# Performance work log

Hardware: AMD Instinct MI355X
Metric: run time of the kernel (lower is better)

## Reference

```python
import jax, jax.numpy as jnp
import numpy as np

B, S, D, F, V, R = 4, 1024, 768, 3072, 2048, 8


def setup_inputs() -> dict:
    key = jax.random.key(0)
    k_x, k_r, k_w1, k_b1, k_w2, k_b2 = jax.random.split(key, 6)
    e_two = jax.random.normal(k_x, (B, S, D), dtype=jnp.float32)
    route_ids = jax.random.randint(k_r, (B, S), 0, R, dtype=jnp.int32)
    # Per-route classification head params (stacked over route axis R).
    W1 = jax.random.normal(k_w1, (R, D, F), dtype=jnp.float32) / np.sqrt(D)
    b1 = jnp.zeros((R, F), dtype=jnp.float32)
    W2 = jax.random.normal(k_w2, (R, F, V), dtype=jnp.float32) / np.sqrt(F)
    b2 = jnp.zeros((R, V), dtype=jnp.float32)
    return {"e_two": e_two, "route_ids": route_ids,
            "W1": W1, "b1": b1, "W2": W2, "b2": b2}


def reference(e_two, route_ids, W1, b1, W2, b2):
    # Each token goes through the MLP classification head selected by its
    # route_id:  softmax(relu(x @ W1[r] + b1[r]) @ W2[r] + b2[r]).
    # Dense formulation: run every route head over all tokens (R is a small
    # fixed set), then gather each token's own route output.
    h = jax.nn.relu(jnp.einsum('bsd,rdf->rbsf', e_two, W1)
                    + b1[:, None, None, :])            # [R,B,S,F]
    logits_all = jnp.einsum('rbsf,rfv->rbsv', h, W2) + b2[:, None, None, :]
    # Select per-token route: [R,B,S,V] -> [B,S,R,V] -> gather along R.
    logits_all = jnp.moveaxis(logits_all, 0, 2)        # [B,S,R,V]
    idx = route_ids[:, :, None, None].astype(jnp.int32)  # [B,S,1,1]
    logits = jnp.take_along_axis(logits_all, idx, axis=2)[:, :, 0, :]  # [B,S,V]
    return jax.nn.softmax(logits, axis=-1)
```

## Files before the change

### kernel.cpp

```cpp
#include <hip/hip_runtime.h>


typedef __attribute__((ext_vector_type(8))) short    s16x8;
typedef __attribute__((ext_vector_type(4))) float    f32x4;

#define T_TOK 4096
#define D_    768
#define F_    3072
#define V_    2048
#define R_    8
#define BM    128
#define BN    128
#define BK    64
#define MAXTILES 40
#define PADROWS  5120

#define OFF_COUNTS  ((size_t)0)
#define OFF_CURS    ((size_t)64)
#define OFF_PADOFF  ((size_t)128)
#define OFF_NT      ((size_t)192)
#define OFF_TROUTE  ((size_t)256)
#define OFF_TROW    ((size_t)1024)
#define OFF_TOK     ((size_t)4096)
#define OFF_XG      ((size_t)32768)
#define OFF_H       (OFF_XG  + (size_t)PADROWS*D_*2)
#define OFF_W1T     (OFF_H   + (size_t)PADROWS*F_*2)
#define OFF_W2T     (OFF_W1T + (size_t)R_*F_*D_*2)

static __device__ __forceinline__ unsigned short f2bf(float f) {
  union { float f; unsigned int u; } x; x.f = f;
  unsigned int r = x.u + 0x7FFFu + ((x.u >> 16) & 1u);
  return (unsigned short)(r >> 16);
}

static __device__ __forceinline__ void gload_lds16(const unsigned short* g,
                                                   unsigned short* l) {
  __builtin_amdgcn_global_load_lds(
      (const __attribute__((address_space(1))) unsigned int*)(const void*)g,
      (__attribute__((address_space(3))) unsigned int*)(void*)l, 16, 0, 0);
}

__global__ void cr_count(const int* __restrict__ route, int* __restrict__ counts) {
  int t = blockIdx.x * blockDim.x + threadIdx.x;
  if (t < T_TOK) atomicAdd(&counts[route[t]], 1);
}

__global__ void cr_plan(const int* __restrict__ counts, int* __restrict__ padOff,
                        int* __restrict__ nTiles, int* __restrict__ tRoute,
                        int* __restrict__ tRow) {
  if (threadIdx.x != 0 || blockIdx.x != 0) return;
  int off = 0, tiles = 0;
  for (int r = 0; r < R_; ++r) {
    padOff[r] = off;
    int nt = (counts[r] + BM - 1) / BM;
    for (int i = 0; i < nt; ++i) { tRoute[tiles] = r; tRow[tiles] = off + i * BM; ++tiles; }
    off += nt * BM;
  }
  padOff[R_] = off;
  *nTiles = tiles;
}

__global__ void cr_scatter(const float* __restrict__ X, const int* __restrict__ route,
                           const int* __restrict__ padOff, int* __restrict__ curs,
                           int* __restrict__ tok, unsigned short* __restrict__ Xg) {
  __shared__ int spos;
  int t = blockIdx.x;
  if (threadIdx.x == 0) {
    int r = route[t];
    int p = padOff[r] + atomicAdd(&curs[r], 1);
    tok[p] = t;
    spos = p;
  }
  __syncthreads();
  int pos = spos;
  float4 v = reinterpret_cast<const float4*>(X + (size_t)t * D_)[threadIdx.x];
  ushort4 o;
  o.x = f2bf(v.x); o.y = f2bf(v.y); o.z = f2bf(v.z); o.w = f2bf(v.w);
  *reinterpret_cast<ushort4*>(Xg + (size_t)pos * D_ + threadIdx.x * 4) = o;
}

template <int K, int N>
__global__ void cr_transpose(const float* __restrict__ W, unsigned short* __restrict__ Wt) {
  __shared__ float tile[128][65];
  int r = blockIdx.z;
  const float* Wr = W + (size_t)r * K * N;
  unsigned short* Wtr = Wt + (size_t)r * N * K;
  int k0 = blockIdx.x * 128, n0 = blockIdx.y * 64;
  int t = threadIdx.x;
  int cb = (t & 15) * 4, rb = t >> 4;
#pragma unroll
  for (int i = 0; i < 8; ++i) {
    int k = rb + i * 16;
    float4 v = *reinterpret_cast<const float4*>(Wr + (size_t)(k0 + k) * N + n0 + cb);
    tile[k][cb] = v.x; tile[k][cb + 1] = v.y; tile[k][cb + 2] = v.z; tile[k][cb + 3] = v.w;
  }
  __syncthreads();
  int nl = t >> 3, kc = (t & 7) * 16;
#pragma unroll
  for (int np = 0; np < 2; ++np) {
    int n = nl + np * 32;
    alignas(16) unsigned short o[16];
#pragma unroll
    for (int j = 0; j < 16; ++j) o[j] = f2bf(tile[kc + j][n]);
    unsigned short* dst = Wtr + (size_t)(n0 + n) * K + k0 + kc;
    *reinterpret_cast<s16x8*>(dst)     = *reinterpret_cast<const s16x8*>(&o[0]);
    *reinterpret_cast<s16x8*>(dst + 8) = *reinterpret_cast<const s16x8*>(&o[8]);
  }
}

template <int K, int N, int MODE, int KSLICES>
__global__ __launch_bounds__(256) void cr_gemm(
    const unsigned short* __restrict__ A, const unsigned short* __restrict__ Wt,
    const float* __restrict__ bias, const int* __restrict__ nTiles,
    const int* __restrict__ tRoute, const int* __restrict__ tRow,
    const int* __restrict__ tok, unsigned short* __restrict__ Hout,
    float* __restrict__ Fout) {
  constexpr int NY = N / BN;
  constexpr int KS_LEN = K / KSLICES;
  int bid = blockIdx.x;
  int ks  = bid / (MAXTILES * NY);
  int rem = bid - ks * (MAXTILES * NY);
  int y   = rem / MAXTILES;
  int mt  = rem - y * MAXTILES;
  if (mt >= *nTiles) return;
  int route = tRoute[mt], row0 = tRow[mt];
  int col0 = y * BN;
  int kbase = ks * KS_LEN;
  const unsigned short* Ag = A + (size_t)row0 * K + kbase;
  const unsigned short* Bg = Wt + ((size_t)route * N + col0) * K + kbase;

  __shared__ __align__(16) unsigned short As[BM * BK];
  __shared__ __align__(16) unsigned short Bs[BN * BK];

  int tid = threadIdx.x, lane = tid & 63, w = tid >> 6;
  int wr = w >> 1, wc = w & 1;
  int rl = lane >> 3;
  int kx = ((lane & 7) ^ rl) * 8;
  int frow = lane & 15;
  int fk   = (lane >> 4) * 8;
  int rx   = (frow & 7) << 3;

  f32x4 acc[4][4] = {};

  for (int kt = 0; kt < KS_LEN; kt += BK) {
#pragma unroll
    for (int j = 0; j < 4; ++j) {
      int c = j * 4 + w;
      gload_lds16(Ag + (size_t)(c * 8 + rl) * K + kt + kx, As + c * 512);
    }
#pragma unroll
    for (int j = 0; j < 4; ++j) {
      int c = j * 4 + w;
      gload_lds16(Bg + (size_t)(c * 8 + rl) * K + kt + kx, Bs + c * 512);
    }
    __syncthreads();
#pragma unroll
    for (int kk = 0; kk < 2; ++kk) {
      s16x8 a[4], b[4];
#pragma unroll
      for (int mi = 0; mi < 4; ++mi)
        a[mi] = *reinterpret_cast<const s16x8*>(
            &As[(wr * 64 + mi * 16 + frow) * BK + ((kk * 32 + fk) ^ rx)]);
#pragma unroll
      for (int ni = 0; ni < 4; ++ni)
        b[ni] = *reinterpret_cast<const s16x8*>(
            &Bs[(wc * 64 + ni * 16 + frow) * BK + ((kk * 32 + fk) ^ rx)]);
#pragma unroll
      for (int mi = 0; mi < 4; ++mi)
#pragma unroll
        for (int ni = 0; ni < 4; ++ni)
          acc[mi][ni] = __builtin_amdgcn_mfma_f32_16x16x32_bf16(
              a[mi], b[ni], acc[mi][ni], 0, 0, 0);
    }
    __syncthreads();
  }

  int crow = (lane >> 4) * 4;
  int ccol = lane & 15;
#pragma unroll
  for (int mi = 0; mi < 4; ++mi) {
#pragma unroll
    for (int ni = 0; ni < 4; ++ni) {
      int gcol = col0 + wc * 64 + ni * 16 + ccol;
#pragma unroll
      for (int j = 0; j < 4; ++j) {
        int prow = row0 + wr * 64 + mi * 16 + crow + j;
        float v = acc[mi][ni][j];
        if (MODE == 0) {
          v = fmaxf(v + bias[(size_t)route * N + gcol], 0.f);
          Hout[(size_t)prow * N + gcol] = f2bf(v);
        } else {
          int tk = tok[prow];
          if (tk >= 0) atomicAdd(&Fout[(size_t)tk * N + gcol], v);
        }
      }
    }
  }
}

__global__ void cr_softmax(float* __restrict__ out, const int* __restrict__ route,
                           const float* __restrict__ b2) {
  int row = blockIdx.x;
  int r = route[row];
  float* p = out + (size_t)row * V_;
  const float* bp = b2 + (size_t)r * V_;
  int t = threadIdx.x;
  float4 v0 = reinterpret_cast<float4*>(p)[t];
  float4 v1 = reinterpret_cast<float4*>(p)[t + 256];
  float4 b0 = reinterpret_cast<const float4*>(bp)[t];
  float4 b1 = reinterpret_cast<const float4*>(bp)[t + 256];
  v0.x += b0.x; v0.y += b0.y; v0.z += b0.z; v0.w += b0.w;
  v1.x += b1.x; v1.y += b1.y; v1.z += b1.z; v1.w += b1.w;
  float m = fmaxf(fmaxf(fmaxf(v0.x, v0.y), fmaxf(v0.z, v0.w)),
                  fmaxf(fmaxf(v1.x, v1.y), fmaxf(v1.z, v1.w)));
#pragma unroll
  for (int o = 32; o; o >>= 1) m = fmaxf(m, __shfl_xor(m, o));
  __shared__ float sm[4], ss[4];
  int w = t >> 6;
  if ((t & 63) == 0) sm[w] = m;
  __syncthreads();
  m = fmaxf(fmaxf(sm[0], sm[1]), fmaxf(sm[2], sm[3]));
  v0.x = expf(v0.x - m); v0.y = expf(v0.y - m); v0.z = expf(v0.z - m); v0.w = expf(v0.w - m);
  v1.x = expf(v1.x - m); v1.y = expf(v1.y - m); v1.z = expf(v1.z - m); v1.w = expf(v1.w - m);
  float s = v0.x + v0.y + v0.z + v0.w + v1.x + v1.y + v1.z + v1.w;
#pragma unroll
  for (int o = 32; o; o >>= 1) s += __shfl_xor(s, o);
  if ((t & 63) == 0) ss[w] = s;
  __syncthreads();
  s = ss[0] + ss[1] + ss[2] + ss[3];
  float inv = 1.f / s;
  v0.x *= inv; v0.y *= inv; v0.z *= inv; v0.w *= inv;
  v1.x *= inv; v1.y *= inv; v1.z *= inv; v1.w *= inv;
  reinterpret_cast<float4*>(p)[t] = v0;
  reinterpret_cast<float4*>(p)[t + 256] = v1;
}

extern "C" void kernel_launch(void* const* d_in, const int* in_sizes, int n_in,
                              void* d_out, int out_size, void* d_ws, size_t ws_size,
                              hipStream_t stream) {
  const float* X      = (const float*)d_in[0];
  const int*   route  = (const int*)d_in[1];
  const float* W1     = (const float*)d_in[2];
  const float* b1     = (const float*)d_in[3];
  const float* W2     = (const float*)d_in[4];
  const float* b2     = (const float*)d_in[5];
  float*       out    = (float*)d_out;
  char*        ws     = (char*)d_ws;

  int* counts = (int*)(ws + OFF_COUNTS);
  int* curs   = (int*)(ws + OFF_CURS);
  int* padOff = (int*)(ws + OFF_PADOFF);
  int* nT     = (int*)(ws + OFF_NT);
  int* tRoute = (int*)(ws + OFF_TROUTE);
  int* tRow   = (int*)(ws + OFF_TROW);
  int* tok    = (int*)(ws + OFF_TOK);
  unsigned short* Xg  = (unsigned short*)(ws + OFF_XG);
  unsigned short* H   = (unsigned short*)(ws + OFF_H);
  unsigned short* W1T = (unsigned short*)(ws + OFF_W1T);
  unsigned short* W2T = (unsigned short*)(ws + OFF_W2T);

  hipMemsetAsync(ws, 0, 4096, stream);
  hipMemsetAsync(ws + OFF_TOK, 0xFF, (size_t)PADROWS * 4, stream);
  hipMemsetAsync(ws + OFF_XG, 0, (size_t)PADROWS * D_ * 2, stream);
  hipMemsetAsync(out, 0, (size_t)T_TOK * V_ * 4, stream);

  cr_count<<<T_TOK / 256, 256, 0, stream>>>(route, counts);
  cr_plan<<<1, 64, 0, stream>>>(counts, padOff, nT, tRoute, tRow);
  cr_scatter<<<T_TOK, 192, 0, stream>>>(X, route, padOff, curs, tok, Xg);

  cr_transpose<D_, F_><<<dim3(D_ / 128, F_ / 64, R_), 256, 0, stream>>>(W1, W1T);
  cr_transpose<F_, V_><<<dim3(F_ / 128, V_ / 64, R_), 256, 0, stream>>>(W2, W2T);

  cr_gemm<D_, F_, 0, 1><<<MAXTILES * (F_ / BN), 256, 0, stream>>>(
      Xg, W1T, b1, nT, tRoute, tRow, tok, H, nullptr);
  cr_gemm<F_, V_, 1, 2><<<MAXTILES * (V_ / BN) * 2, 256, 0, stream>>>(
      H, W2T, nullptr, nT, tRoute, tRow, tok, nullptr, out);

  cr_softmax<<<T_TOK, 256, 0, stream>>>(out, route, b2);
}
```

Baseline: 639.9 us.

## Double-buffer GEMM LDS tiles and drop split-K atomics for direct stores

```diff
diff --git a/kernel.cpp b/kernel.cpp
--- a/kernel.cpp
+++ b/kernel.cpp
@@ -108,29 +108,25 @@
   }
 }
 
-template <int K, int N, int MODE, int KSLICES>
+template <int K, int N, int MODE>
 __global__ __launch_bounds__(256) void cr_gemm(
     const unsigned short* __restrict__ A, const unsigned short* __restrict__ Wt,
     const float* __restrict__ bias, const int* __restrict__ nTiles,
     const int* __restrict__ tRoute, const int* __restrict__ tRow,
     const int* __restrict__ tok, unsigned short* __restrict__ Hout,
     float* __restrict__ Fout) {
-  constexpr int NY = N / BN;
-  constexpr int KS_LEN = K / KSLICES;
+  constexpr int NSTEP = K / BK;
   int bid = blockIdx.x;
-  int ks  = bid / (MAXTILES * NY);
-  int rem = bid - ks * (MAXTILES * NY);
-  int y   = rem / MAXTILES;
-  int mt  = rem - y * MAXTILES;
+  int y   = bid / MAXTILES;
+  int mt  = bid - y * MAXTILES;
   if (mt >= *nTiles) return;
   int route = tRoute[mt], row0 = tRow[mt];
   int col0 = y * BN;
-  int kbase = ks * KS_LEN;
-  const unsigned short* Ag = A + (size_t)row0 * K + kbase;
-  const unsigned short* Bg = Wt + ((size_t)route * N + col0) * K + kbase;
-
-  __shared__ __align__(16) unsigned short As[BM * BK];
-  __shared__ __align__(16) unsigned short Bs[BN * BK];
+  const unsigned short* Ag = A + (size_t)row0 * K;
+  const unsigned short* Bg = Wt + ((size_t)route * N + col0) * K;
+
+  __shared__ __align__(16) unsigned short As[2][BM * BK];
+  __shared__ __align__(16) unsigned short Bs[2][BN * BK];
 
   int tid = threadIdx.x, lane = tid & 63, w = tid >> 6;
   int wr = w >> 1, wc = w & 1;
@@ -142,29 +138,30 @@
 
   f32x4 acc[4][4] = {};
 
-  for (int kt = 0; kt < KS_LEN; kt += BK) {
+  auto stage = [&](int buf, int kt) {
 #pragma unroll
     for (int j = 0; j < 4; ++j) {
       int c = j * 4 + w;
-      gload_lds16(Ag + (size_t)(c * 8 + rl) * K + kt + kx, As + c * 512);
+      gload_lds16(Ag + (size_t)(c * 8 + rl) * K + kt + kx, &As[buf][c * 512]);
     }
 #pragma unroll
     for (int j = 0; j < 4; ++j) {
       int c = j * 4 + w;
-      gload_lds16(Bg + (size_t)(c * 8 + rl) * K + kt + kx, Bs + c * 512);
-    }
-    __syncthreads();
+      gload_lds16(Bg + (size_t)(c * 8 + rl) * K + kt + kx, &Bs[buf][c * 512]);
+    }
+  };
+  auto compute = [&](int buf) {
 #pragma unroll
     for (int kk = 0; kk < 2; ++kk) {
       s16x8 a[4], b[4];
 #pragma unroll
       for (int mi = 0; mi < 4; ++mi)
         a[mi] = *reinterpret_cast<const s16x8*>(
-            &As[(wr * 64 + mi * 16 + frow) * BK + ((kk * 32 + fk) ^ rx)]);
+            &As[buf][(wr * 64 + mi * 16 + frow) * BK + ((kk * 32 + fk) ^ rx)]);
 #pragma unroll
       for (int ni = 0; ni < 4; ++ni)
         b[ni] = *reinterpret_cast<const s16x8*>(
-            &Bs[(wc * 64 + ni * 16 + frow) * BK + ((kk * 32 + fk) ^ rx)]);
+            &Bs[buf][(wc * 64 + ni * 16 + frow) * BK + ((kk * 32 + fk) ^ rx)]);
 #pragma unroll
       for (int mi = 0; mi < 4; ++mi)
 #pragma unroll
@@ -172,7 +169,22 @@
           acc[mi][ni] = __builtin_amdgcn_mfma_f32_16x16x32_bf16(
               a[mi], b[ni], acc[mi][ni], 0, 0, 0);
     }
-    __syncthreads();
+  };
+
+  stage(0, 0);
+  for (int t = 0; t < NSTEP; ++t) {
+    int buf = t & 1;
+    if (t + 1 < NSTEP) {
+      stage(buf ^ 1, (t + 1) * BK);
+      asm volatile("s_waitcnt vmcnt(8)" ::: "memory");
+    } else {
+      asm volatile("s_waitcnt vmcnt(0)" ::: "memory");
+    }
+    __builtin_amdgcn_s_barrier();
+    __builtin_amdgcn_sched_barrier(0);
+    compute(buf);
+    __builtin_amdgcn_sched_barrier(0);
+    __builtin_amdgcn_s_barrier();
   }
 
   int crow = (lane >> 4) * 4;
@@ -182,35 +194,28 @@
 #pragma unroll
     for (int ni = 0; ni < 4; ++ni) {
       int gcol = col0 + wc * 64 + ni * 16 + ccol;
+      float bv = bias[(size_t)route * N + gcol];
 #pragma unroll
       for (int j = 0; j < 4; ++j) {
         int prow = row0 + wr * 64 + mi * 16 + crow + j;
-        float v = acc[mi][ni][j];
+        float v = acc[mi][ni][j] + bv;
         if (MODE == 0) {
-          v = fmaxf(v + bias[(size_t)route * N + gcol], 0.f);
-          Hout[(size_t)prow * N + gcol] = f2bf(v);
+          Hout[(size_t)prow * N + gcol] = f2bf(fmaxf(v, 0.f));
         } else {
           int tk = tok[prow];
-          if (tk >= 0) atomicAdd(&Fout[(size_t)tk * N + gcol], v);
+          if (tk >= 0) Fout[(size_t)tk * N + gcol] = v;
         }
       }
     }
   }
 }
 
-__global__ void cr_softmax(float* __restrict__ out, const int* __restrict__ route,
-                           const float* __restrict__ b2) {
+__global__ void cr_softmax(float* __restrict__ out) {
   int row = blockIdx.x;
-  int r = route[row];
   float* p = out + (size_t)row * V_;
-  const float* bp = b2 + (size_t)r * V_;
   int t = threadIdx.x;
   float4 v0 = reinterpret_cast<float4*>(p)[t];
   float4 v1 = reinterpret_cast<float4*>(p)[t + 256];
-  float4 b0 = reinterpret_cast<const float4*>(bp)[t];
-  float4 b1 = reinterpret_cast<const float4*>(bp)[t + 256];
-  v0.x += b0.x; v0.y += b0.y; v0.z += b0.z; v0.w += b0.w;
-  v1.x += b1.x; v1.y += b1.y; v1.z += b1.z; v1.w += b1.w;
   float m = fmaxf(fmaxf(fmaxf(v0.x, v0.y), fmaxf(v0.z, v0.w)),
                   fmaxf(fmaxf(v1.x, v1.y), fmaxf(v1.z, v1.w)));
 #pragma unroll
@@ -262,7 +267,6 @@
   hipMemsetAsync(ws, 0, 4096, stream);
   hipMemsetAsync(ws + OFF_TOK, 0xFF, (size_t)PADROWS * 4, stream);
   hipMemsetAsync(ws + OFF_XG, 0, (size_t)PADROWS * D_ * 2, stream);
-  hipMemsetAsync(out, 0, (size_t)T_TOK * V_ * 4, stream);
 
   cr_count<<<T_TOK / 256, 256, 0, stream>>>(route, counts);
   cr_plan<<<1, 64, 0, stream>>>(counts, padOff, nT, tRoute, tRow);
@@ -271,10 +275,10 @@
   cr_transpose<D_, F_><<<dim3(D_ / 128, F_ / 64, R_), 256, 0, stream>>>(W1, W1T);
   cr_transpose<F_, V_><<<dim3(F_ / 128, V_ / 64, R_), 256, 0, stream>>>(W2, W2T);
 
-  cr_gemm<D_, F_, 0, 1><<<MAXTILES * (F_ / BN), 256, 0, stream>>>(
+  cr_gemm<D_, F_, 0><<<MAXTILES * (F_ / BN), 256, 0, stream>>>(
       Xg, W1T, b1, nT, tRoute, tRow, tok, H, nullptr);
-  cr_gemm<F_, V_, 1, 2><<<MAXTILES * (V_ / BN) * 2, 256, 0, stream>>>(
-      H, W2T, nullptr, nT, tRoute, tRow, tok, nullptr, out);
-
-  cr_softmax<<<T_TOK, 256, 0, stream>>>(out, route, b2);
-}
+  cr_gemm<F_, V_, 1><<<MAXTILES * (V_ / BN), 256, 0, stream>>>(
+      H, W2T, b2, nT, tRoute, tRow, tok, nullptr, out);
+
+  cr_softmax<<<T_TOK, 256, 0, stream>>>(out);
+}
```

After: 622.3 us. 2.8% less time.
